# Kernel optimization log

Measured on AMD Instinct MI355X. Metric: run time of the kernel, lower is better.

Reference implementation:

```python
import jax, jax.numpy as jnp
import numpy as np

EMBED_DIM = 768
NUM_HEADS = 12
D_K = EMBED_DIM // NUM_HEADS


def setup_inputs() -> dict:
    key = jax.random.key(0)
    ks = jax.random.split(key, 9)
    b, s, d = 4, 2048, EMBED_DIM
    scale = 1.0 / np.sqrt(d)
    x = jax.random.normal(ks[0], (b, s, d), dtype=jnp.float32)
    return {
        "x": x,
        "w_q": jax.random.normal(ks[1], (d, d), dtype=jnp.float32) * scale,
        "b_q": jnp.zeros((d,), dtype=jnp.float32),
        "w_k": jax.random.normal(ks[2], (d, d), dtype=jnp.float32) * scale,
        "b_k": jnp.zeros((d,), dtype=jnp.float32),
        "w_v": jax.random.normal(ks[3], (d, d), dtype=jnp.float32) * scale,
        "b_v": jnp.zeros((d,), dtype=jnp.float32),
        "w_o": jax.random.normal(ks[4], (d, d), dtype=jnp.float32) * scale,
        "b_o": jnp.zeros((d,), dtype=jnp.float32),
    }


def reference(x, w_q, b_q, w_k, b_k, w_v, b_v, w_o, b_o):
    b, s, d = x.shape
    h, dk = NUM_HEADS, D_K
    # projections (torch Linear: x @ W^T + b)
    q = (x @ w_q.T + b_q).reshape(b, s, h, dk).transpose(0, 2, 1, 3)
    k = (x @ w_k.T + b_k).reshape(b, s, h, dk).transpose(0, 2, 1, 3)
    v = (x @ w_v.T + b_v).reshape(b, s, h, dk).transpose(0, 2, 1, 3)
    # causal attention: full [b,h,s,s] scores as in the original
    scores = jnp.einsum("bhqd,bhkd->bhqk", q, k) / jnp.sqrt(jnp.float32(dk))
    causal = jnp.tril(jnp.ones((s, s), dtype=bool))
    scores = jnp.where(causal[None, None], scores, -jnp.inf)
    attn = jax.nn.softmax(scores, axis=-1)
    out = jnp.einsum("bhqk,bhkd->bhqd", attn, v)
    out = out.transpose(0, 2, 1, 3).reshape(b, s, h * dk)
    return out @ w_o.T + b_o
```

## Files before the change

kernel.cpp:

```cpp
#include <hip/hip_runtime.h>
#include <hip/hip_bf16.h>
#include <stdint.h>

typedef short bf16x8 __attribute__((ext_vector_type(8)));
typedef float f32x4 __attribute__((ext_vector_type(4)));
typedef unsigned short u16;


__device__ __forceinline__ u16 f2bf_bits(float f) {
    __hip_bfloat16 h = __float2bfloat16(f);
    return __builtin_bit_cast(u16, h);
}

__device__ __forceinline__ uint32_t pack2bf(float a, float b) {
    uint32_t ua = __builtin_bit_cast(uint32_t, a) + 0x8000u;
    uint32_t ub = __builtin_bit_cast(uint32_t, b) + 0x8000u;
    return __builtin_amdgcn_perm(ub, ua, 0x07060302u);
}

__device__ __forceinline__ void gld_lds16(const void* g, void* l) {
    __builtin_amdgcn_global_load_lds(
        (const __attribute__((address_space(1))) void*)g,
        (__attribute__((address_space(3))) void*)l, 16, 0, 0);
}

#define CEXP 0.18033688011112042f


__global__ __launch_bounds__(256) void cast_all_kernel(
    const float* __restrict__ x, const float* __restrict__ w0,
    const float* __restrict__ w1, const float* __restrict__ w2,
    const float* __restrict__ w3, u16* __restrict__ xb,
    u16* __restrict__ o0, u16* __restrict__ o1,
    u16* __restrict__ o2, u16* __restrict__ o3,
    const float* __restrict__ bq, const float* __restrict__ bk,
    const float* __restrict__ bv, float* __restrict__ biasf) {
    int gid = blockIdx.x * 256 + threadIdx.x;
    const float* s;
    u16* d;
    int off;
    if (gid < 1572864) {
        s = x; d = xb; off = gid;
    } else {
        int g2 = gid - 1572864;
        int which = g2 / 147456;
        off = g2 - which * 147456;
        s = which == 0 ? w0 : which == 1 ? w1 : which == 2 ? w2 : w3;
        d = which == 0 ? o0 : which == 1 ? o1 : which == 2 ? o2 : o3;
    }
    float4 v = ((const float4*)s)[off];
    ushort4 u;
    u.x = f2bf_bits(v.x); u.y = f2bf_bits(v.y);
    u.z = f2bf_bits(v.z); u.w = f2bf_bits(v.w);
    ((ushort4*)d)[off] = u;
    if (gid < 2304) {
        float bb = gid < 768 ? bq[gid] : gid < 1536 ? bk[gid - 768] : bv[gid - 1536];
        biasf[gid] = bb;
    }
}


template <int RT, int MODE>
__global__ __launch_bounds__(256) void gemm_xwt(
    const u16* __restrict__ X, const u16* __restrict__ W,
    const float* __restrict__ bias, float* __restrict__ Cf,
    u16* __restrict__ Cb, u16* __restrict__ Vt, int K, int NC) {
    constexpr int JR = RT / 32;
    __shared__ u16 lsX[RT * 64];
    __shared__ u16 lsW[128 * 64];
    const int tid = threadIdx.x;
    const int w = tid >> 6, lane = tid & 63;
    const int quad = lane >> 4, l15 = lane & 15;
    const int m0 = blockIdx.y * RT, n0 = blockIdx.x * 128;
    const int wr = (w >> 1) * (RT / 2), wc = (w & 1) * 64;
    const int rr = lane >> 3, c8 = lane & 7;

    f32x4 acc[JR][4];
    for (int j = 0; j < JR; ++j)
        for (int i = 0; i < 4; ++i) acc[j][i] = (f32x4){0.f, 0.f, 0.f, 0.f};

    const int KT = K / 64;
    for (int kt = 0; kt < KT; ++kt) {
        const int k0 = kt * 64;
        __syncthreads();
        for (int cb = w; cb < RT / 8; cb += 4) {
            int row = cb * 8 + rr;
            int cg = c8 ^ ((rr ^ cb) & 7);
            gld_lds16(X + (size_t)(m0 + row) * K + k0 + cg * 8, &lsX[cb * 512]);
        }
        for (int cb = w; cb < 16; cb += 4) {
            int row = cb * 8 + rr;
            int cg = c8 ^ ((rr ^ cb) & 7);
            gld_lds16(W + (size_t)(n0 + row) * K + k0 + cg * 8, &lsW[cb * 512]);
        }
        __syncthreads();

        for (int kk = 0; kk < 2; ++kk) {
            bf16x8 xf[JR], wf[4];
            for (int j = 0; j < JR; ++j) {
                int row = wr + j * 16 + l15;
                int slot = (kk * 4 + quad) ^ ((row ^ (row >> 3)) & 7);
                xf[j] = *(const bf16x8*)&lsX[row * 64 + slot * 8];
            }
            for (int i = 0; i < 4; ++i) {
                int row = wc + i * 16 + l15;
                int slot = (kk * 4 + quad) ^ ((row ^ (row >> 3)) & 7);
                wf[i] = *(const bf16x8*)&lsW[row * 64 + slot * 8];
            }
            for (int j = 0; j < JR; ++j)
                for (int i = 0; i < 4; ++i)
                    acc[j][i] = __builtin_amdgcn_mfma_f32_16x16x32_bf16(
                        wf[i], xf[j], acc[j][i], 0, 0, 0);
        }
    }

    const bool vtile = (MODE == 2) && (n0 >= 1536);
    for (int i = 0; i < 4; ++i) {
        int c0 = n0 + wc + i * 16 + quad * 4;
        float4 bv4 = *(const float4*)&bias[c0];
        for (int j = 0; j < JR; ++j) {
            int row = m0 + wr + j * 16 + l15;
            float v0 = acc[j][i][0] + bv4.x;
            float v1 = acc[j][i][1] + bv4.y;
            float v2 = acc[j][i][2] + bv4.z;
            float v3 = acc[j][i][3] + bv4.w;
            if (MODE == 1) {
                float4 o4 = {v0, v1, v2, v3};
                *(float4*)&Cf[(size_t)row * NC + c0] = o4;
            } else if (vtile) {
                int d = c0 - 1536;
                int bq_ = row >> 11;
                int s = row & 2047;
                int h = d >> 6, dd = d & 63;
                size_t base = ((size_t)(bq_ * 12 + h) * 64 + dd) * 2048 + s;
                Vt[base]          = f2bf_bits(v0);
                Vt[base + 2048]   = f2bf_bits(v1);
                Vt[base + 4096]   = f2bf_bits(v2);
                Vt[base + 6144]   = f2bf_bits(v3);
            } else {
                uint2 pk = {pack2bf(v0, v1), pack2bf(v2, v3)};
                *(uint2*)&Cb[(size_t)row * NC + c0] = pk;
            }
        }
    }
}


__global__ __launch_bounds__(256, 3) void attn_kernel(
    const u16* __restrict__ QKV, const u16* __restrict__ Vt, u16* __restrict__ O) {
    __shared__ u16 lsQ[128 * 64];
    __shared__ u16 lsK0[64 * 64];
    __shared__ u16 lsV0[64 * 64];
    __shared__ u16 lsP[4][32 * 72];

    int bx = blockIdx.x;
    int bh = bx % 48;
    int j  = bx / 48;
    const int ta = j;
    const int tb = 31 - j;
    int bb = bh / 12, h = bh % 12;
    int tid = threadIdx.x, w = tid >> 6, lane = tid & 63;
    int quad = lane >> 4, l15 = lane & 15;
    int rr = lane >> 3, c8 = lane & 7;

    u16* K1 = lsQ;
    u16* V1 = lsQ + 4096;

    const size_t kgbase = (size_t)(bb * 2048) * 2304 + 768 + (size_t)h * 64;
    const size_t vgbase = (size_t)(bh * 64) * 2048;

    auto stage = [&](int kt, u16* lsK, u16* lsV) {
        for (int cb = w; cb < 8; cb += 4) {
            int row = cb * 8 + rr;
            int cg = c8 ^ ((rr ^ cb) & 7);
            gld_lds16(QKV + kgbase + (size_t)(kt * 64 + row) * 2304 + cg * 8,
                      &lsK[cb * 512]);
            gld_lds16(Vt + vgbase + (size_t)row * 2048 + kt * 64 + cg * 8,
                      &lsV[cb * 512]);
        }
    };

    for (int cb = w; cb < 16; cb += 4) {
        int row = cb * 8 + rr;
        int qrow = (row < 64) ? ta * 64 + row : tb * 64 + (row - 64);
        int cg = c8 ^ ((rr ^ cb) & 7);
        gld_lds16(QKV + (size_t)(bb * 2048 + qrow) * 2304 + h * 64 + cg * 8,
                  &lsQ[cb * 512]);
    }
    stage(0, lsK0, lsV0);
    __syncthreads();

    bf16x8 q0[2], q1[2];
    for (int g = 0; g < 2; ++g) {
        int rowq = g * 64 + w * 16 + l15;
        int swq = (rowq ^ (rowq >> 3)) & 7;
        q0[g] = *(const bf16x8*)&lsQ[rowq * 64 + ((0 + quad) ^ swq) * 8];
        q1[g] = *(const bf16x8*)&lsQ[rowq * 64 + ((4 + quad) ^ swq) * 8];
    }
    __syncthreads();

    f32x4 oacc0[4], oacc1[4];
    for (int dt = 0; dt < 4; ++dt) {
        oacc0[dt] = (f32x4){0.f, 0.f, 0.f, 0.f};
        oacc1[dt] = (f32x4){0.f, 0.f, 0.f, 0.f};
    }
    float li0 = 0.f, li1 = 0.f;
    u16* Pw = lsP[w];
    const int qrel = w * 16 + l15;

    auto compute = [&](int kt, const u16* lsK, const u16* lsV) {
        const bool do0 = (kt <= ta);

        f32x4 S0[4], S1[4];
        __builtin_amdgcn_s_setprio(1);
        for (int ct = 0; ct < 4; ++ct) {
            int rowk = ct * 16 + l15;
            int swk = (rowk ^ (rowk >> 3)) & 7;
            bf16x8 k0 = *(const bf16x8*)&lsK[rowk * 64 + ((0 + quad) ^ swk) * 8];
            bf16x8 k1 = *(const bf16x8*)&lsK[rowk * 64 + ((4 + quad) ^ swk) * 8];
            f32x4 z = (f32x4){0.f, 0.f, 0.f, 0.f};
            S1[ct] = __builtin_amdgcn_mfma_f32_16x16x32_bf16(k0, q0[1], z, 0, 0, 0);
            S1[ct] = __builtin_amdgcn_mfma_f32_16x16x32_bf16(k1, q1[1], S1[ct], 0, 0, 0);
            if (do0) {
                S0[ct] = __builtin_amdgcn_mfma_f32_16x16x32_bf16(k0, q0[0], z, 0, 0, 0);
                S0[ct] = __builtin_amdgcn_mfma_f32_16x16x32_bf16(k1, q1[0], S0[ct], 0, 0, 0);
            }
        }
        __builtin_amdgcn_s_setprio(0);

        if (kt == ta) {
            for (int ct = 0; ct < 4; ++ct) {
                int kbase = ct * 16 + quad * 4;
                for (int r = 0; r < 4; ++r)
                    if (kbase + r > qrel) S0[ct][r] = -1e30f;
            }
        }
        if (kt == tb) {
            for (int ct = 0; ct < 4; ++ct) {
                int kbase = ct * 16 + quad * 4;
                for (int r = 0; r < 4; ++r)
                    if (kbase + r > qrel) S1[ct][r] = -1e30f;
            }
        }

        if (do0) {
            u16* Pr = &Pw[(size_t)l15 * 72];
            for (int ct = 0; ct < 4; ++ct) {
                float p0 = __builtin_amdgcn_exp2f(S0[ct][0] * CEXP);
                float p1 = __builtin_amdgcn_exp2f(S0[ct][1] * CEXP);
                float p2 = __builtin_amdgcn_exp2f(S0[ct][2] * CEXP);
                float p3 = __builtin_amdgcn_exp2f(S0[ct][3] * CEXP);
                li0 += (p0 + p1) + (p2 + p3);
                uint2 pk = {pack2bf(p0, p1), pack2bf(p2, p3)};
                *(uint2*)&Pr[ct * 16 + quad * 4] = pk;
            }
        }
        {
            u16* Pr = &Pw[(size_t)(16 + l15) * 72];
            for (int ct = 0; ct < 4; ++ct) {
                float p0 = __builtin_amdgcn_exp2f(S1[ct][0] * CEXP);
                float p1 = __builtin_amdgcn_exp2f(S1[ct][1] * CEXP);
                float p2 = __builtin_amdgcn_exp2f(S1[ct][2] * CEXP);
                float p3 = __builtin_amdgcn_exp2f(S1[ct][3] * CEXP);
                li1 += (p0 + p1) + (p2 + p3);
                uint2 pk = {pack2bf(p0, p1), pack2bf(p2, p3)};
                *(uint2*)&Pr[ct * 16 + quad * 4] = pk;
            }
        }

        __builtin_amdgcn_s_setprio(1);
        for (int ks = 0; ks < 2; ++ks) {
            bf16x8 bp1 = *(const bf16x8*)&Pw[(size_t)(16 + l15) * 72 + ks * 32 + quad * 8];
            bf16x8 bp0;
            if (do0) bp0 = *(const bf16x8*)&Pw[(size_t)l15 * 72 + ks * 32 + quad * 8];
            for (int dt = 0; dt < 4; ++dt) {
                int rowv = dt * 16 + l15;
                int swv = (rowv ^ (rowv >> 3)) & 7;
                bf16x8 av = *(const bf16x8*)&lsV[rowv * 64 + ((ks * 4 + quad) ^ swv) * 8];
                oacc1[dt] = __builtin_amdgcn_mfma_f32_16x16x32_bf16(av, bp1, oacc1[dt], 0, 0, 0);
                if (do0)
                    oacc0[dt] = __builtin_amdgcn_mfma_f32_16x16x32_bf16(av, bp0, oacc0[dt], 0, 0, 0);
            }
        }
        __builtin_amdgcn_s_setprio(0);
    };

    for (int kt = 0; kt + 1 <= tb; kt += 2) {
        stage(kt + 1, K1, V1);
        compute(kt, lsK0, lsV0);
        __syncthreads();
        if (kt + 2 <= tb) stage(kt + 2, lsK0, lsV0);
        compute(kt + 1, K1, V1);
        __syncthreads();
    }
    if ((tb & 1) == 0) compute(tb, lsK0, lsV0);

    li0 += __shfl_xor(li0, 16, 64);
    li0 += __shfl_xor(li0, 32, 64);
    li1 += __shfl_xor(li1, 16, 64);
    li1 += __shfl_xor(li1, 32, 64);
    float inv0 = 1.0f / li0, inv1 = 1.0f / li1;

    for (int g = 0; g < 2; ++g) {
        float inv = g ? inv1 : inv0;
        f32x4* oa = g ? oacc1 : oacc0;
        int row = (g ? tb : ta) * 64 + w * 16 + l15;
        for (int dt = 0; dt < 4; ++dt) {
            uint2 pk = {pack2bf(oa[dt][0] * inv, oa[dt][1] * inv),
                        pack2bf(oa[dt][2] * inv, oa[dt][3] * inv)};
            *(uint2*)&O[(size_t)(bb * 2048 + row) * 768 + h * 64 + dt * 16 + quad * 4] = pk;
        }
    }
}


extern "C" void kernel_launch(void* const* d_in, const int* in_sizes, int n_in,
                              void* d_out, int out_size, void* d_ws, size_t ws_size,
                              hipStream_t stream) {
    const float* x  = (const float*)d_in[0];
    const float* wq = (const float*)d_in[1];
    const float* bq = (const float*)d_in[2];
    const float* wk = (const float*)d_in[3];
    const float* bk = (const float*)d_in[4];
    const float* wv = (const float*)d_in[5];
    const float* bv = (const float*)d_in[6];
    const float* wo = (const float*)d_in[7];
    const float* bo = (const float*)d_in[8];
    float* out = (float*)d_out;

    char* ws = (char*)d_ws;
    u16*   xb    = (u16*)(ws + 0);
    u16*   Wf    = (u16*)(ws + 12582912);
    u16*   wob   = (u16*)(ws + 16121856);
    float* biasf = (float*)(ws + 17301504);
    u16*   QKVb  = (u16*)(ws + 17310720);
    u16*   Vtw   = (u16*)(ws + 55059456);
    u16*   Ow    = (u16*)(ws + 67642368);

    cast_all_kernel<<<8448, 256, 0, stream>>>(x, wq, wk, wv, wo,
                                              xb, Wf, Wf + 589824, Wf + 1179648, wob,
                                              bq, bk, bv, biasf);

    gemm_xwt<128, 2><<<dim3(18, 64), 256, 0, stream>>>(xb, Wf, biasf, nullptr, QKVb,
                                                       Vtw, 768, 2304);
    attn_kernel<<<768, 256, 0, stream>>>(QKVb, Vtw, Ow);
    gemm_xwt<64, 1><<<dim3(6, 128), 256, 0, stream>>>(Ow, wob, bo, out, nullptr,
                                                      nullptr, 768, 768);
}
```

Measured before the change: 205.5 us.

## Double-buffer GEMM LDS tiles and remap blocks across XCDs

The projection and output GEMMs now use two LDS buffers. The global-to-LDS load of the next K-tile is issued before the MFMA work on the current tile, so load latency overlaps compute and one barrier per step is removed. The 2D grid becomes 1D, and block IDs are remapped so consecutive output tiles land on the same XCD, which should improve L2 reuse of the shared X and W rows. In exchange, LDS use per block doubles, which may lower occupancy. The loop also assumes an even number of K-tiles.

```diff
diff --git a/kernel.cpp b/kernel.cpp
--- a/kernel.cpp
+++ b/kernel.cpp
@@ -64,14 +64,17 @@
 __global__ __launch_bounds__(256) void gemm_xwt(
     const u16* __restrict__ X, const u16* __restrict__ W,
     const float* __restrict__ bias, float* __restrict__ Cf,
-    u16* __restrict__ Cb, u16* __restrict__ Vt, int K, int NC) {
+    u16* __restrict__ Cb, u16* __restrict__ Vt, int K, int NC, int NTIL) {
     constexpr int JR = RT / 32;
-    __shared__ u16 lsX[RT * 64];
-    __shared__ u16 lsW[128 * 64];
+    __shared__ u16 lsX[2 * RT * 64];
+    __shared__ u16 lsW[2 * 128 * 64];
     const int tid = threadIdx.x;
     const int w = tid >> 6, lane = tid & 63;
     const int quad = lane >> 4, l15 = lane & 15;
-    const int m0 = blockIdx.y * RT, n0 = blockIdx.x * 128;
+    const int cpx = gridDim.x >> 3;
+    const int sb = (blockIdx.x & 7) * cpx + (blockIdx.x >> 3);
+    const int mt = sb / NTIL, nt = sb - mt * NTIL;
+    const int m0 = mt * RT, n0 = nt * 128;
     const int wr = (w >> 1) * (RT / 2), wc = (w & 1) * 64;
     const int rr = lane >> 3, c8 = lane & 7;
 
@@ -79,39 +82,54 @@
     for (int j = 0; j < JR; ++j)
         for (int i = 0; i < 4; ++i) acc[j][i] = (f32x4){0.f, 0.f, 0.f, 0.f};
 
-    const int KT = K / 64;
-    for (int kt = 0; kt < KT; ++kt) {
+    auto stage = [&](int kt, int buf) {
         const int k0 = kt * 64;
-        __syncthreads();
+        u16* dX = lsX + buf * (RT * 64);
+        u16* dW = lsW + buf * (128 * 64);
         for (int cb = w; cb < RT / 8; cb += 4) {
             int row = cb * 8 + rr;
             int cg = c8 ^ ((rr ^ cb) & 7);
-            gld_lds16(X + (size_t)(m0 + row) * K + k0 + cg * 8, &lsX[cb * 512]);
+            gld_lds16(X + (size_t)(m0 + row) * K + k0 + cg * 8, &dX[cb * 512]);
         }
         for (int cb = w; cb < 16; cb += 4) {
             int row = cb * 8 + rr;
             int cg = c8 ^ ((rr ^ cb) & 7);
-            gld_lds16(W + (size_t)(n0 + row) * K + k0 + cg * 8, &lsW[cb * 512]);
-        }
-        __syncthreads();
-
+            gld_lds16(W + (size_t)(n0 + row) * K + k0 + cg * 8, &dW[cb * 512]);
+        }
+    };
+
+    auto compute = [&](int buf) {
+        const u16* sX = lsX + buf * (RT * 64);
+        const u16* sW = lsW + buf * (128 * 64);
         for (int kk = 0; kk < 2; ++kk) {
             bf16x8 xf[JR], wf[4];
             for (int j = 0; j < JR; ++j) {
                 int row = wr + j * 16 + l15;
                 int slot = (kk * 4 + quad) ^ ((row ^ (row >> 3)) & 7);
-                xf[j] = *(const bf16x8*)&lsX[row * 64 + slot * 8];
+                xf[j] = *(const bf16x8*)&sX[row * 64 + slot * 8];
             }
             for (int i = 0; i < 4; ++i) {
                 int row = wc + i * 16 + l15;
                 int slot = (kk * 4 + quad) ^ ((row ^ (row >> 3)) & 7);
-                wf[i] = *(const bf16x8*)&lsW[row * 64 + slot * 8];
+                wf[i] = *(const bf16x8*)&sW[row * 64 + slot * 8];
             }
             for (int j = 0; j < JR; ++j)
                 for (int i = 0; i < 4; ++i)
                     acc[j][i] = __builtin_amdgcn_mfma_f32_16x16x32_bf16(
                         wf[i], xf[j], acc[j][i], 0, 0, 0);
         }
+    };
+
+    const int KT = K / 64;
+    stage(0, 0);
+    __syncthreads();
+    for (int kt = 0; kt < KT; kt += 2) {
+        stage(kt + 1, 1);
+        compute(0);
+        __syncthreads();
+        if (kt + 2 < KT) stage(kt + 2, 0);
+        compute(1);
+        __syncthreads();
     }
 
     const bool vtile = (MODE == 2) && (n0 >= 1536);
@@ -341,9 +359,9 @@
                                               xb, Wf, Wf + 589824, Wf + 1179648, wob,
                                               bq, bk, bv, biasf);
 
-    gemm_xwt<128, 2><<<dim3(18, 64), 256, 0, stream>>>(xb, Wf, biasf, nullptr, QKVb,
-                                                       Vtw, 768, 2304);
+    gemm_xwt<128, 2><<<1152, 256, 0, stream>>>(xb, Wf, biasf, nullptr, QKVb,
+                                               Vtw, 768, 2304, 18);
     attn_kernel<<<768, 256, 0, stream>>>(QKVb, Vtw, Ow);
-    gemm_xwt<64, 1><<<dim3(6, 128), 256, 0, stream>>>(Ow, wob, bo, out, nullptr,
-                                                      nullptr, 768, 768);
-}
+    gemm_xwt<64, 1><<<768, 256, 0, stream>>>(Ow, wob, bo, out, nullptr,
+                                             nullptr, 768, 768, 6);
+}
```

After: 216.4 us. +5.3%, slower.
